# Kernel optimization log

Hardware: AMD Instinct MI355X
Metric: run time of the kernel (lower is better)

The kernel has to match this reference:

```python
import jax, jax.numpy as jnp
import numpy as np

B, S, H, NH, DH, F, L = 4, 2048, 512, 8, 64, 2048, 4
ALPHA = 1.0   # config.lag_time_scale_alpha
EPS = 1e-12   # BERT layer_norm_eps
MS_PER_MIN = 60.0 * 1000.0


def setup_inputs() -> dict:
    key = jax.random.key(0)
    ks = jax.random.split(key, 24)
    p = lambda k, shape: (jax.random.normal(k, shape, jnp.float32) * 0.02)
    inp = {
        "query_states": jax.random.normal(ks[0], (B, S, H), jnp.float32),
        "attention_mask": jnp.zeros((B, 1, 1, S), jnp.float32),
        "position_bias": jax.random.normal(ks[1], (1, NH, S, S), jnp.float32) * 0.02,
        "timestamp": jnp.sort(jax.random.randint(ks[2], (B, S), 0, 36_000_000, jnp.int32), axis=-1),
        # stacked per-layer parameters (L leading dim)
        "wq": p(ks[3], (L, H, H)), "bq": jnp.zeros((L, H), jnp.float32),
        "wk": p(ks[4], (L, H, H)), "bk": jnp.zeros((L, H), jnp.float32),
        "wv": p(ks[5], (L, H, H)), "bv": jnp.zeros((L, H), jnp.float32),
        "wo": p(ks[6], (L, H, H)), "bo": jnp.zeros((L, H), jnp.float32),
        "ln1_g": jnp.ones((L, H), jnp.float32), "ln1_b": jnp.zeros((L, H), jnp.float32),
        "wi": p(ks[7], (L, H, F)), "bi": jnp.zeros((L, F), jnp.float32),
        "wo2": p(ks[8], (L, F, H)), "bo2": jnp.zeros((L, H), jnp.float32),
        "ln2_g": jnp.ones((L, H), jnp.float32), "ln2_b": jnp.zeros((L, H), jnp.float32),
    }
    return inp


def _ln(x, g, b):
    m = x.mean(-1, keepdims=True)
    v = ((x - m) ** 2).mean(-1, keepdims=True)
    return (x - m) / jnp.sqrt(v + EPS) * g + b


def reference(query_states, attention_mask, position_bias, timestamp,
              wq, bq, wk, bk, wv, bv, wo, bo, ln1_g, ln1_b,
              wi, bi, wo2, bo2, ln2_g, ln2_b):
    # encoder (is_decoder=False) lag-time scale: (B,1,S,S)
    lag = (timestamp[:, None, :, None] - timestamp[:, None, None, :]).astype(jnp.float32) / MS_PER_MIN
    scale = np.sqrt(DH).astype(np.float32) - ALPHA / (jnp.clip(lag, 0.0) + 1.0) + ALPHA

    x = query_states
    for l in range(L):
        def proj(w, b):
            return (x @ w + b).reshape(B, S, NH, DH).transpose(0, 2, 1, 3)  # (B,NH,S,DH)
        q, k, v = proj(wq[l], bq[l]), proj(wk[l], bk[l]), proj(wv[l], bv[l])
        scores = jnp.einsum('bhqd,bhkd->bhqk', q, k) / scale + position_bias + attention_mask
        probs = jax.nn.softmax(scores, axis=-1)
        ctx = jnp.einsum('bhqk,bhkd->bhqd', probs, v).transpose(0, 2, 1, 3).reshape(B, S, H)
        attn = _ln(ctx @ wo[l] + bo[l] + x, ln1_g[l], ln1_b[l])
        ffn = jax.nn.gelu(attn @ wi[l] + bi[l], approximate=False) @ wo2[l] + bo2[l]
        x = _ln(ffn + attn, ln2_g[l], ln2_b[l])
    return x
```

## Files before the change

kernel.cpp:

```cpp
#include <hip/hip_runtime.h>
#include <stdint.h>

typedef unsigned short u16;
using half8   = __attribute__((ext_vector_type(8))) _Float16;
using float4v = __attribute__((ext_vector_type(4))) float;

#define L2E 1.4426950408889634f

__device__ inline float4v f4zero() { float4v z = {0.f, 0.f, 0.f, 0.f}; return z; }

__device__ inline u16 f2h(float f) {
  union { _Float16 h; u16 u; } v; v.h = (_Float16)f; return v.u;
}
__device__ inline float h2f(u16 u) {
  union { u16 u; _Float16 h; } v; v.u = u; return (float)v.h;
}

__device__ inline void glds16(const u16* g, u16* lds_base, int lane) {
#if __has_builtin(__builtin_amdgcn_global_load_lds)
  (void)lane;
  __builtin_amdgcn_global_load_lds((const __attribute__((address_space(1))) void*)g,
                                   (__attribute__((address_space(3))) void*)lds_base,
                                   16, 0, 0);
#else
  *(uint4*)(lds_base + (size_t)lane * 8) = *(const uint4*)g;
#endif
}

__global__ __launch_bounds__(256) void transpose_cast_kernel(
    const float* __restrict__ in, u16* __restrict__ out, int K, int N, size_t out_ls) {
  __shared__ float tile[32][33];
  const int tx = threadIdx.x & 31, ty = threadIdx.x >> 5;
  in  += (size_t)blockIdx.z * K * N;
  out += (size_t)blockIdx.z * out_ls;
  const int n  = blockIdx.x * 32 + tx;
  const int k0 = blockIdx.y * 32;
#pragma unroll
  for (int j = 0; j < 32; j += 8)
    tile[ty + j][tx] = in[(size_t)(k0 + ty + j) * N + n];
  __syncthreads();
  const int k = k0 + tx;
  const int n0 = blockIdx.x * 32;
#pragma unroll
  for (int j = 0; j < 32; j += 8)
    out[(size_t)(n0 + ty + j) * K + k] = f2h(tile[tx][ty + j]);
}

__global__ __launch_bounds__(256) void cast_kernel(const float* __restrict__ in,
                                                   u16* __restrict__ out) {
  const int i = (blockIdx.x * 256 + threadIdx.x) * 4;
  float4 t = *(const float4*)(in + i);
  ushort4 o;
  o.x = f2h(t.x); o.y = f2h(t.y); o.z = f2h(t.z); o.w = f2h(t.w);
  *(ushort4*)(out + i) = o;
}

__global__ __launch_bounds__(256) void pb_tile_kernel(const float* __restrict__ pb,
                                                      u16* __restrict__ pbT) {
  const int g  = blockIdx.x * 256 + threadIdx.x;
  const int mm = g & 15;
  const int q  = (g >> 4) & 2047;
  const int kbh = g >> 15;
  const int kb = kbh & 31, h = kbh >> 5;
  const float* src = pb + ((size_t)h * 2048 + q) * 2048 + kb * 64 + mm;
  ushort4 o;
  o.x = f2h(src[0]  * L2E);
  o.y = f2h(src[16] * L2E);
  o.z = f2h(src[32] * L2E);
  o.w = f2h(src[48] * L2E);
  *(ushort4*)(pbT + ((size_t)(h * 32 + kb) * 2048 + q) * 64 + mm * 4) = o;
}

__global__ __launch_bounds__(256) void inv_tile_kernel(const int* __restrict__ ts,
                                                       u16* __restrict__ invT) {
  const int g  = blockIdx.x * 256 + threadIdx.x;
  const int mm = g & 15;
  const int q  = (g >> 4) & 2047;
  const int kb = (g >> 15) & 31;
  const int b  = g >> 20;
  const int tq = ts[b * 2048 + q];
  ushort4 o;
  u16* op = (u16*)&o;
#pragma unroll
  for (int nb = 0; nb < 4; nb++) {
    const int k = kb * 64 + nb * 16 + mm;
    const int du = tq - ts[b * 2048 + k];
    const float u = (du > 0) ? (float)du : 0.f;
    op[nb] = f2h(fmaf(u, L2E, 86561.70245333781f) *
                 __builtin_amdgcn_rcpf(fmaf(u, 9.f, 480000.f)));
  }
  *(ushort4*)(invT + ((size_t)(b * 32 + kb) * 2048 + q) * 64 + mm * 4) = o;
}

__global__ __launch_bounds__(256) void maskts_kernel(const float* __restrict__ mask,
                                                     const int* __restrict__ ts,
                                                     float* __restrict__ maskE,
                                                     float* __restrict__ tsf) {
  const int i = blockIdx.x * 256 + threadIdx.x;
  maskE[i] = mask[i] * L2E;
  tsf[i]   = (float)ts[i];
}

template <int BM, int BN, int NN, int KK, int EPI>
__global__ __launch_bounds__(256) void gemm_kernel(
    const u16* __restrict__ A, const u16* __restrict__ Wt,
    const float* __restrict__ b0, const float* __restrict__ b1, const float* __restrict__ b2,
    const u16* __restrict__ resid,
    void* __restrict__ o0, void* __restrict__ o1, void* __restrict__ o2) {
  constexpr int FI = BM / 32;
  constexpr int FJB = BN / 32;
  constexpr int FIW = BM / 32;
  constexpr int FJW = BN / 32;
  __shared__ __align__(16) u16 As[BM * 64];
  __shared__ __align__(16) u16 Bs[BN * 64];
  const int tid = threadIdx.x, lane = tid & 63, wv = tid >> 6;
  const int quad = lane >> 4, mm = lane & 15;
  const int m0 = blockIdx.x * BM, n0 = blockIdx.y * BN;
  const int wm = (wv >> 1) * (BM / 2), wn = (wv & 1) * (BN / 2);
  const int srow = tid >> 3, slot = tid & 7;
  const int chunk = slot ^ (srow & 7);
  const u16* Ag = A  + (size_t)(m0 + srow) * KK + chunk * 8;
  const u16* Bg = Wt + (size_t)(n0 + srow) * KK + chunk * 8;
  u16* AsW = As + (size_t)(wv * 8) * 64;
  u16* BsW = Bs + (size_t)(wv * 8) * 64;
  const int sw = mm & 7;

  float4v acc[FIW][FJW];
#pragma unroll
  for (int i = 0; i < FIW; i++)
#pragma unroll
    for (int j = 0; j < FJW; j++) acc[i][j] = f4zero();

  for (int kt = 0; kt < KK; kt += 64) {
#pragma unroll
    for (int i = 0; i < FI; i++)
      glds16(Ag + (size_t)i * 32 * KK + kt, AsW + i * 32 * 64, lane);
#pragma unroll
    for (int j = 0; j < FJB; j++)
      glds16(Bg + (size_t)j * 32 * KK + kt, BsW + j * 32 * 64, lane);
    __syncthreads();
#pragma unroll
    for (int ks = 0; ks < 2; ks++) {
      half8 a[FIW], b[FJW];
#pragma unroll
      for (int i = 0; i < FIW; i++)
        a[i] = *(const half8*)(As + (size_t)(wm + i * 16 + mm) * 64 + (size_t)((ks * 4 + quad) ^ sw) * 8);
#pragma unroll
      for (int j = 0; j < FJW; j++)
        b[j] = *(const half8*)(Bs + (size_t)(wn + j * 16 + mm) * 64 + (size_t)((ks * 4 + quad) ^ sw) * 8);
#pragma unroll
      for (int i = 0; i < FIW; i++)
#pragma unroll
        for (int j = 0; j < FJW; j++)
          acc[i][j] = __builtin_amdgcn_mfma_f32_16x16x32_f16(a[i], b[j], acc[i][j], 0, 0, 0);
    }
    __syncthreads();
  }

#pragma unroll
  for (int j = 0; j < FJW; j++) {
    const int gn = n0 + wn + j * 16 + mm;
    if (EPI == 4) {
      const int which = gn >> 9, col = gn & 511, h = (gn >> 6) & 7, d = gn & 63;
      const float* bp = (which == 0) ? b0 : (which == 1) ? b1 : b2;
      const float bias = bp[col];
      u16* dst = (which == 0) ? (u16*)o0 : (which == 1) ? (u16*)o1 : (u16*)o2;
#pragma unroll
      for (int i = 0; i < FIW; i++)
#pragma unroll
        for (int r = 0; r < 4; r++) {
          const int gm = m0 + wm + i * 16 + quad * 4 + r;
          const int b_ = gm >> 11, s_ = gm & 2047;
          const float val = acc[i][j][r] + bias;
          if (which < 2)
            dst[((size_t)((b_ * 8 + h) * 2048 + s_)) * 64 + d] = f2h(val);
          else
            dst[((size_t)((b_ * 8 + h) * 64 + d)) * 2048 + s_] = f2h(val);
        }
    } else {
      const float bias = b0[gn];
#pragma unroll
      for (int i = 0; i < FIW; i++)
#pragma unroll
        for (int r = 0; r < 4; r++) {
          const int gm = m0 + wm + i * 16 + quad * 4 + r;
          const float val = acc[i][j][r] + bias;
          const size_t idx = (size_t)gm * NN + gn;
          if (EPI == 2) {
            ((float*)o0)[idx] = val + h2f(resid[idx]);
          } else {
            const float z  = val * 0.70710678118654752f;
            const float az = fabsf(z);
            const float t  = __builtin_amdgcn_rcpf(1.0f + 0.3275911f * az);
            const float poly = t * (0.254829592f + t * (-0.284496736f +
                               t * (1.421413741f + t * (-1.453152027f + t * 1.061405429f))));
            const float e = __builtin_amdgcn_exp2f(-az * az * L2E);
            float erf_ = 1.0f - poly * e;
            erf_ = (z < 0.0f) ? -erf_ : erf_;
            ((u16*)o0)[idx] = f2h(val * 0.5f * (1.0f + erf_));
          }
        }
    }
  }
}

template <int TILED>
__global__ __launch_bounds__(256) void flash4_kernel(
    const u16* __restrict__ Q, const u16* __restrict__ Kb, const u16* __restrict__ Vt,
    const u16* __restrict__ pbT, const u16* __restrict__ invT,
    const float* __restrict__ pb32,
    const float* __restrict__ maskE, const float* __restrict__ tsf,
    u16* __restrict__ ctx) {
  __shared__ __align__(16) u16 Kls[64 * 64];
  __shared__ __align__(16) u16 Vls[64 * 64];
  __shared__ __align__(16) u16 P[4][16 * 72];
  const int tid = threadIdx.x, lane = tid & 63, w = tid >> 6;
  const int quad = lane >> 4, mm = lane & 15;
  const int bh = blockIdx.y, b_ = bh >> 3, h_ = bh & 7;
  const int q0 = blockIdx.x * 64 + w * 16;
  const size_t qk_base = (size_t)bh * 2048 * 64;
  const size_t v_base  = (size_t)bh * 64 * 2048;
  const int srow = lane >> 3, slot = lane & 7;
  const int chunk = slot ^ srow;
  const int sw = mm & 7;

  half8 aq[2];
#pragma unroll
  for (int t = 0; t < 2; t++)
    aq[t] = *(const half8*)(Q + qk_base + (size_t)(q0 + mm) * 64 + t * 32 + quad * 8);

  float tqf[4];
  if (TILED < 2) {
#pragma unroll
    for (int r = 0; r < 4; r++) tqf[r] = tsf[b_ * 2048 + q0 + quad * 4 + r];
  }

  float l_r[4] = {0.f, 0.f, 0.f, 0.f};
  float4v o[4];
#pragma unroll
  for (int ob = 0; ob < 4; ob++) o[ob] = f4zero();

  ushort4 pbc[4], invc[4]; float tkc[4], mkc[4];
  if (TILED >= 1) {
#pragma unroll
    for (int r = 0; r < 4; r++)
      pbc[r] = *(const ushort4*)(pbT + ((size_t)(h_ * 32) * 2048 + q0 + quad * 4 + r) * 64 + mm * 4);
  }
  if (TILED == 2) {
#pragma unroll
    for (int r = 0; r < 4; r++)
      invc[r] = *(const ushort4*)(invT + ((size_t)(b_ * 32) * 2048 + q0 + quad * 4 + r) * 64 + mm * 4);
  } else {
#pragma unroll
    for (int nb = 0; nb < 4; nb++) tkc[nb] = tsf[b_ * 2048 + nb * 16 + mm];
  }
#pragma unroll
  for (int nb = 0; nb < 4; nb++) mkc[nb] = maskE[b_ * 2048 + nb * 16 + mm];

  for (int kt = 0; kt < 32; kt++) {
    const int k0 = kt * 64;
    __syncthreads();
#pragma unroll
    for (int i = 0; i < 2; i++) {
      const int row = w * 16 + i * 8 + srow;
      glds16(Kb + qk_base + (size_t)(k0 + row) * 64 + chunk * 8, Kls + (w * 16 + i * 8) * 64, lane);
      glds16(Vt + v_base + (size_t)row * 2048 + k0 + chunk * 8, Vls + (w * 16 + i * 8) * 64, lane);
    }
    __syncthreads();

    float4v s[4];
#pragma unroll
    for (int nb = 0; nb < 4; nb++) {
      const half8 kf0 = *(const half8*)(Kls + (size_t)(nb * 16 + mm) * 64 + (size_t)(quad ^ sw) * 8);
      const half8 kf1 = *(const half8*)(Kls + (size_t)(nb * 16 + mm) * 64 + (size_t)((4 + quad) ^ sw) * 8);
      s[nb] = __builtin_amdgcn_mfma_f32_16x16x32_f16(aq[0], kf0, f4zero(), 0, 0, 0);
      s[nb] = __builtin_amdgcn_mfma_f32_16x16x32_f16(aq[1], kf1, s[nb], 0, 0, 0);
    }

    const int kn = (kt < 31) ? kt + 1 : kt;
    ushort4 pbn[4], invn[4]; float tkn[4], mkn[4];
    if (TILED >= 1) {
#pragma unroll
      for (int r = 0; r < 4; r++)
        pbn[r] = *(const ushort4*)(pbT + ((size_t)(h_ * 32 + kn) * 2048 + q0 + quad * 4 + r) * 64 + mm * 4);
    }
    if (TILED == 2) {
#pragma unroll
      for (int r = 0; r < 4; r++)
        invn[r] = *(const ushort4*)(invT + ((size_t)(b_ * 32 + kn) * 2048 + q0 + quad * 4 + r) * 64 + mm * 4);
    } else {
#pragma unroll
      for (int nb = 0; nb < 4; nb++) tkn[nb] = tsf[b_ * 2048 + kn * 64 + nb * 16 + mm];
    }
#pragma unroll
    for (int nb = 0; nb < 4; nb++) mkn[nb] = maskE[b_ * 2048 + kn * 64 + nb * 16 + mm];

#pragma unroll
    for (int r = 0; r < 4; r++) {
      float pbv[4], iv[4];
      if (TILED >= 1) {
        pbv[0] = h2f(pbc[r].x); pbv[1] = h2f(pbc[r].y);
        pbv[2] = h2f(pbc[r].z); pbv[3] = h2f(pbc[r].w);
      } else {
#pragma unroll
        for (int nb = 0; nb < 4; nb++)
          pbv[nb] = pb32[((size_t)h_ * 2048 + q0 + quad * 4 + r) * 2048 + k0 + nb * 16 + mm] * L2E;
      }
      if (TILED == 2) {
        iv[0] = h2f(invc[r].x); iv[1] = h2f(invc[r].y);
        iv[2] = h2f(invc[r].z); iv[3] = h2f(invc[r].w);
      } else {
#pragma unroll
        for (int nb = 0; nb < 4; nb++) {
          const float u = fmaxf(tqf[r] - tkc[nb], 0.f);
          iv[nb] = fmaf(u, L2E, 86561.70245333781f) *
                   __builtin_amdgcn_rcpf(fmaf(u, 9.f, 480000.f));
        }
      }
#pragma unroll
      for (int nb = 0; nb < 4; nb++) {
        const float t = fmaf(s[nb][r], iv[nb], pbv[nb] + mkc[nb]);
        const float p = __builtin_amdgcn_exp2f(t);
        l_r[r] += p;
        P[w][(quad * 4 + r) * 72 + nb * 16 + mm] = f2h(p);
      }
    }

    const half8 ap0 = *(const half8*)(&P[w][mm * 72 + quad * 8]);
    const half8 ap1 = *(const half8*)(&P[w][mm * 72 + 32 + quad * 8]);
#pragma unroll
    for (int ob = 0; ob < 4; ob++) {
      const half8 vf0 = *(const half8*)(Vls + (size_t)(ob * 16 + mm) * 64 + (size_t)(quad ^ sw) * 8);
      const half8 vf1 = *(const half8*)(Vls + (size_t)(ob * 16 + mm) * 64 + (size_t)((4 + quad) ^ sw) * 8);
      o[ob] = __builtin_amdgcn_mfma_f32_16x16x32_f16(ap0, vf0, o[ob], 0, 0, 0);
      o[ob] = __builtin_amdgcn_mfma_f32_16x16x32_f16(ap1, vf1, o[ob], 0, 0, 0);
    }
#pragma unroll
    for (int r = 0; r < 4; r++) { pbc[r] = pbn[r]; invc[r] = invn[r]; }
#pragma unroll
    for (int nb = 0; nb < 4; nb++) { tkc[nb] = tkn[nb]; mkc[nb] = mkn[nb]; }
  }

#pragma unroll
  for (int r = 0; r < 4; r++) {
    float l = l_r[r];
#pragma unroll
    for (int sh = 1; sh < 16; sh <<= 1) l += __shfl_xor(l, sh, 64);
    const float rl = __builtin_amdgcn_rcpf(l);
    const int qrow = q0 + quad * 4 + r;
#pragma unroll
    for (int ob = 0; ob < 4; ob++)
      ctx[((size_t)b_ * 2048 + qrow) * 512 + h_ * 64 + ob * 16 + mm] = f2h(o[ob][r] * rl);
  }
}

__global__ __launch_bounds__(256) void ln_kernel(
    const float* __restrict__ in, const float* __restrict__ g, const float* __restrict__ bb,
    float* __restrict__ of, u16* __restrict__ obf) {
  const int lane = threadIdx.x & 63, w = threadIdx.x >> 6;
  const int row = blockIdx.x * 4 + w;
  const float* x = in + (size_t)row * 512;
  float v[8];
  const float4 t0 = *(const float4*)(x + lane * 8);
  const float4 t1 = *(const float4*)(x + lane * 8 + 4);
  v[0] = t0.x; v[1] = t0.y; v[2] = t0.z; v[3] = t0.w;
  v[4] = t1.x; v[5] = t1.y; v[6] = t1.z; v[7] = t1.w;
  float s = 0.f;
#pragma unroll
  for (int i = 0; i < 8; i++) s += v[i];
#pragma unroll
  for (int sh = 1; sh < 64; sh <<= 1) s += __shfl_xor(s, sh, 64);
  const float mean = s * (1.0f / 512.0f);
  float sq = 0.f;
#pragma unroll
  for (int i = 0; i < 8; i++) { const float d = v[i] - mean; sq += d * d; }
#pragma unroll
  for (int sh = 1; sh < 64; sh <<= 1) sq += __shfl_xor(sq, sh, 64);
  const float rstd = rsqrtf(sq * (1.0f / 512.0f) + 1e-12f);
#pragma unroll
  for (int i = 0; i < 8; i++) {
    const int col = lane * 8 + i;
    const float y = (v[i] - mean) * rstd * g[col] + bb[col];
    if (of) of[(size_t)row * 512 + col] = y;
    obf[(size_t)row * 512 + col] = f2h(y);
  }
}

extern "C" void kernel_launch(void* const* d_in, const int* in_sizes, int n_in,
                              void* d_out, int out_size, void* d_ws, size_t ws_size,
                              hipStream_t stream) {
  const float* x_in = (const float*)d_in[0];
  const float* mask = (const float*)d_in[1];
  const float* pb   = (const float*)d_in[2];
  const int*   ts   = (const int*)d_in[3];
  const float* wq = (const float*)d_in[4];  const float* bq = (const float*)d_in[5];
  const float* wk = (const float*)d_in[6];  const float* bk = (const float*)d_in[7];
  const float* wvp = (const float*)d_in[8]; const float* bv = (const float*)d_in[9];
  const float* wo = (const float*)d_in[10]; const float* bo = (const float*)d_in[11];
  const float* ln1g = (const float*)d_in[12]; const float* ln1b = (const float*)d_in[13];
  const float* wi = (const float*)d_in[14]; const float* bi = (const float*)d_in[15];
  const float* wo2 = (const float*)d_in[16]; const float* bo2 = (const float*)d_in[17];
  const float* ln2g = (const float*)d_in[18]; const float* ln2b = (const float*)d_in[19];

  char* ws = (char*)d_ws;
  const size_t o_wqkv  = 0;
  const size_t o_woT   = 6291456;
  const size_t o_wiT   = 8388608;
  const size_t o_wo2T  = 16777216;
  const size_t o_maskE = 25165824;
  const size_t o_tsf   = 25198592;
  const size_t o_xbf   = 25231360;
  const size_t o_qb    = 33619968;
  const size_t o_kb    = 42008576;
  const size_t o_vb    = 50397184;
  const size_t o_ctx   = 58785792;
  const size_t o_attnb = 67174400;
  const size_t o_tmp   = 75563008;
  const size_t o_pbT   = 92340224;
  const size_t o_invT  = 159449088;
  const int tiled = (ws_size >= o_invT + 33554432ull) ? 2
                  : (ws_size >= o_pbT + 67108864ull) ? 1 : 0;

  u16*   wqkvT = (u16*)(ws + o_wqkv);
  u16*   woT   = (u16*)(ws + o_woT);
  u16*   wiT   = (u16*)(ws + o_wiT);
  u16*   wo2T  = (u16*)(ws + o_wo2T);
  float* maskE = (float*)(ws + o_maskE);
  float* tsf   = (float*)(ws + o_tsf);
  u16*   xbf   = (u16*)(ws + o_xbf);
  u16*   qb    = (u16*)(ws + o_qb);
  u16*   kb    = (u16*)(ws + o_kb);
  u16*   vb    = (u16*)(ws + o_vb);
  u16*   ctx   = (u16*)(ws + o_ctx);
  u16*   hb    = (u16*)(ws + o_qb);
  u16*   attnb = (u16*)(ws + o_attnb);
  float* tmp   = (float*)(ws + o_tmp);
  u16*   pbT   = (u16*)(ws + o_pbT);
  u16*   invT  = (u16*)(ws + o_invT);

  const dim3 blk(256);
  transpose_cast_kernel<<<dim3(16, 16, 4), blk, 0, stream>>>(wq,  wqkvT,          512, 512, 786432);
  transpose_cast_kernel<<<dim3(16, 16, 4), blk, 0, stream>>>(wk,  wqkvT + 262144, 512, 512, 786432);
  transpose_cast_kernel<<<dim3(16, 16, 4), blk, 0, stream>>>(wvp, wqkvT + 524288, 512, 512, 786432);
  transpose_cast_kernel<<<dim3(16, 16, 4), blk, 0, stream>>>(wo,  woT,  512, 512,  262144);
  transpose_cast_kernel<<<dim3(64, 16, 4), blk, 0, stream>>>(wi,  wiT,  512, 2048, 1048576);
  transpose_cast_kernel<<<dim3(16, 64, 4), blk, 0, stream>>>(wo2, wo2T, 2048, 512, 1048576);
  maskts_kernel<<<32, blk, 0, stream>>>(mask, ts, maskE, tsf);
  cast_kernel<<<4096, blk, 0, stream>>>(x_in, xbf);
  if (tiled >= 1) pb_tile_kernel<<<32768, blk, 0, stream>>>(pb, pbT);
  if (tiled == 2) inv_tile_kernel<<<16384, blk, 0, stream>>>(ts, invT);

  for (int l = 0; l < 4; l++) {
    gemm_kernel<128, 128, 1536, 512, 4><<<dim3(64, 12), blk, 0, stream>>>(
        xbf, wqkvT + (size_t)l * 786432, bq + l * 512, bk + l * 512, bv + l * 512,
        nullptr, qb, kb, vb);
    if (tiled == 2)
      flash4_kernel<2><<<dim3(32, 32), blk, 0, stream>>>(qb, kb, vb, pbT, invT, pb, maskE, tsf, ctx);
    else if (tiled == 1)
      flash4_kernel<1><<<dim3(32, 32), blk, 0, stream>>>(qb, kb, vb, pbT, nullptr, pb, maskE, tsf, ctx);
    else
      flash4_kernel<0><<<dim3(32, 32), blk, 0, stream>>>(qb, kb, vb, nullptr, nullptr, pb, maskE, tsf, ctx);
    gemm_kernel<128, 64, 512, 512, 2><<<dim3(64, 8), blk, 0, stream>>>(
        ctx, woT + (size_t)l * 262144, bo + l * 512, nullptr, nullptr, xbf,
        tmp, nullptr, nullptr);
    ln_kernel<<<2048, blk, 0, stream>>>(tmp, ln1g + l * 512, ln1b + l * 512, nullptr, attnb);
    gemm_kernel<128, 128, 2048, 512, 3><<<dim3(64, 16), blk, 0, stream>>>(
        attnb, wiT + (size_t)l * 1048576, bi + l * 2048, nullptr, nullptr, nullptr,
        hb, nullptr, nullptr);
    gemm_kernel<128, 64, 512, 2048, 2><<<dim3(64, 8), blk, 0, stream>>>(
        hb, wo2T + (size_t)l * 1048576, bo2 + l * 512, nullptr, nullptr, attnb,
        tmp, nullptr, nullptr);
    ln_kernel<<<2048, blk, 0, stream>>>(tmp, ln2g + l * 512, ln2b + l * 512,
                                        (l == 3) ? (float*)d_out : nullptr, xbf);
  }
  (void)in_sizes; (void)n_in; (void)out_size;
}
```

Baseline: 1.368 ms.

## Double-buffer flash attention and output GEMMs, fragment-ordered bias tiles, fp16 residual temp

The flash attention kernel now double-buffers its K/V LDS tiles so the next tile's global loads overlap the current tile's compute, and it drops one of the two barriers per iteration. Position-bias and lag-scale tiles are pre-laid out in MFMA fragment order so each lane reads two 16-byte vectors per tile. The P scratch uses an XOR swizzle in place of padding. A new double-buffered GEMM handles the output and FFN-down projections and writes the residual sum in fp16, which halves the LayerNorm input traffic at some cost in precision. The intermediate tiled=1 path is also removed.

```diff
diff --git a/kernel.cpp b/kernel.cpp
--- a/kernel.cpp
+++ b/kernel.cpp
@@ -27,6 +27,11 @@
 #endif
 }
 
+__device__ inline void wave_fence_barrier() {
+  __asm__ volatile("s_waitcnt vmcnt(0) lgkmcnt(0)" ::: "memory");
+  __builtin_amdgcn_s_barrier();
+}
+
 __global__ __launch_bounds__(256) void transpose_cast_kernel(
     const float* __restrict__ in, u16* __restrict__ out, int K, int N, size_t out_ls) {
   __shared__ float tile[32][33];
@@ -55,41 +60,54 @@
   *(ushort4*)(out + i) = o;
 }
 
-__global__ __launch_bounds__(256) void pb_tile_kernel(const float* __restrict__ pb,
-                                                      u16* __restrict__ pbT) {
-  const int g  = blockIdx.x * 256 + threadIdx.x;
-  const int mm = g & 15;
-  const int q  = (g >> 4) & 2047;
-  const int kbh = g >> 15;
-  const int kb = kbh & 31, h = kbh >> 5;
-  const float* src = pb + ((size_t)h * 2048 + q) * 2048 + kb * 64 + mm;
-  ushort4 o;
-  o.x = f2h(src[0]  * L2E);
-  o.y = f2h(src[16] * L2E);
-  o.z = f2h(src[32] * L2E);
-  o.w = f2h(src[48] * L2E);
-  *(ushort4*)(pbT + ((size_t)(h * 32 + kb) * 2048 + q) * 64 + mm * 4) = o;
-}
-
-__global__ __launch_bounds__(256) void inv_tile_kernel(const int* __restrict__ ts,
-                                                       u16* __restrict__ invT) {
-  const int g  = blockIdx.x * 256 + threadIdx.x;
-  const int mm = g & 15;
-  const int q  = (g >> 4) & 2047;
-  const int kb = (g >> 15) & 31;
-  const int b  = g >> 20;
-  const int tq = ts[b * 2048 + q];
-  ushort4 o;
-  u16* op = (u16*)&o;
-#pragma unroll
-  for (int nb = 0; nb < 4; nb++) {
+__global__ __launch_bounds__(256) void pb_tile2_kernel(const float* __restrict__ pb,
+                                                       u16* __restrict__ pbT) {
+  const int g    = blockIdx.x * 256 + threadIdx.x;
+  const int half = g & 1;
+  const int lane = (g >> 1) & 63;
+  const int qg   = (g >> 7) & 127;
+  const int kb   = (g >> 14) & 31;
+  const int h    = g >> 19;
+  const int quad = lane >> 4, mm = lane & 15;
+  ushort4 o[2];
+  u16* op = (u16*)o;
+#pragma unroll
+  for (int e = 0; e < 8; e++) {
+    const int nb = half * 2 + (e >> 2), r = e & 3;
+    const int q = qg * 16 + quad * 4 + r;
     const int k = kb * 64 + nb * 16 + mm;
-    const int du = tq - ts[b * 2048 + k];
+    op[e] = f2h(pb[((size_t)h * 2048 + q) * 2048 + k] * L2E);
+  }
+  *(uint4*)(pbT + ((((size_t)h * 32 + kb) * 128 + qg) * 64 + lane) * 16 + half * 8) =
+      *(uint4*)o;
+}
+
+__global__ __launch_bounds__(256) void inv_tile2_kernel(const int* __restrict__ ts,
+                                                        u16* __restrict__ invT) {
+  const int g    = blockIdx.x * 256 + threadIdx.x;
+  const int half = g & 1;
+  const int lane = (g >> 1) & 63;
+  const int qg   = (g >> 7) & 127;
+  const int kb   = (g >> 14) & 31;
+  const int b    = g >> 19;
+  const int quad = lane >> 4, mm = lane & 15;
+  int tq[4], tk[2];
+#pragma unroll
+  for (int r = 0; r < 4; r++) tq[r] = ts[b * 2048 + qg * 16 + quad * 4 + r];
+#pragma unroll
+  for (int n = 0; n < 2; n++) tk[n] = ts[b * 2048 + kb * 64 + (half * 2 + n) * 16 + mm];
+  ushort4 o[2];
+  u16* op = (u16*)o;
+#pragma unroll
+  for (int e = 0; e < 8; e++) {
+    const int n = e >> 2, r = e & 3;
+    const int du = tq[r] - tk[n];
     const float u = (du > 0) ? (float)du : 0.f;
-    op[nb] = f2h(fmaf(u, L2E, 86561.70245333781f) *
-                 __builtin_amdgcn_rcpf(fmaf(u, 9.f, 480000.f)));
-  }
-  *(ushort4*)(invT + ((size_t)(b * 32 + kb) * 2048 + q) * 64 + mm * 4) = o;
+    op[e] = f2h(fmaf(u, L2E, 86561.70245333781f) *
+                __builtin_amdgcn_rcpf(fmaf(u, 9.f, 480000.f)));
+  }
+  *(uint4*)(invT + ((((size_t)b * 32 + kb) * 128 + qg) * 64 + lane) * 16 + half * 8) =
+      *(uint4*)o;
 }
 
 __global__ __launch_bounds__(256) void maskts_kernel(const float* __restrict__ mask,
@@ -105,7 +123,6 @@
 __global__ __launch_bounds__(256) void gemm_kernel(
     const u16* __restrict__ A, const u16* __restrict__ Wt,
     const float* __restrict__ b0, const float* __restrict__ b1, const float* __restrict__ b2,
-    const u16* __restrict__ resid,
     void* __restrict__ o0, void* __restrict__ o1, void* __restrict__ o2) {
   constexpr int FI = BM / 32;
   constexpr int FJB = BN / 32;
@@ -186,38 +203,110 @@
           const int gm = m0 + wm + i * 16 + quad * 4 + r;
           const float val = acc[i][j][r] + bias;
           const size_t idx = (size_t)gm * NN + gn;
-          if (EPI == 2) {
-            ((float*)o0)[idx] = val + h2f(resid[idx]);
-          } else {
-            const float z  = val * 0.70710678118654752f;
-            const float az = fabsf(z);
-            const float t  = __builtin_amdgcn_rcpf(1.0f + 0.3275911f * az);
-            const float poly = t * (0.254829592f + t * (-0.284496736f +
-                               t * (1.421413741f + t * (-1.453152027f + t * 1.061405429f))));
-            const float e = __builtin_amdgcn_exp2f(-az * az * L2E);
-            float erf_ = 1.0f - poly * e;
-            erf_ = (z < 0.0f) ? -erf_ : erf_;
-            ((u16*)o0)[idx] = f2h(val * 0.5f * (1.0f + erf_));
-          }
+          const float z  = val * 0.70710678118654752f;
+          const float az = fabsf(z);
+          const float t  = __builtin_amdgcn_rcpf(1.0f + 0.3275911f * az);
+          const float poly = t * (0.254829592f + t * (-0.284496736f +
+                             t * (1.421413741f + t * (-1.453152027f + t * 1.061405429f))));
+          const float e = __builtin_amdgcn_exp2f(-az * az * L2E);
+          float erf_ = 1.0f - poly * e;
+          erf_ = (z < 0.0f) ? -erf_ : erf_;
+          ((u16*)o0)[idx] = f2h(val * 0.5f * (1.0f + erf_));
         }
     }
   }
 }
 
+template <int KK>
+__global__ __launch_bounds__(256) void gemm_db_kernel(
+    const u16* __restrict__ A, const u16* __restrict__ Wt,
+    const float* __restrict__ b0, const u16* __restrict__ resid,
+    u16* __restrict__ out) {
+  constexpr int KT = KK / 64;
+  __shared__ __align__(16) u16 As[2][128 * 64];
+  __shared__ __align__(16) u16 Bs[2][64 * 64];
+  const int tid = threadIdx.x, lane = tid & 63, wv = tid >> 6;
+  const int quad = lane >> 4, mm = lane & 15;
+  const int m0 = blockIdx.x * 128, n0 = blockIdx.y * 64;
+  const int wm = (wv >> 1) * 64, wn = (wv & 1) * 32;
+  const int srow = tid >> 3, slot = tid & 7;
+  const int chunk = slot ^ (srow & 7);
+  const u16* Ag = A  + (size_t)(m0 + srow) * KK + chunk * 8;
+  const u16* Bg = Wt + (size_t)(n0 + srow) * KK + chunk * 8;
+  const int woff = (wv * 8) * 64;
+  const int sw = mm & 7;
+
+  float4v acc[4][2];
+#pragma unroll
+  for (int i = 0; i < 4; i++)
+#pragma unroll
+    for (int j = 0; j < 2; j++) acc[i][j] = f4zero();
+
+#pragma unroll
+  for (int i = 0; i < 4; i++) glds16(Ag + (size_t)i * 32 * KK, As[0] + woff + i * 32 * 64, lane);
+#pragma unroll
+  for (int j = 0; j < 2; j++) glds16(Bg + (size_t)j * 32 * KK, Bs[0] + woff + j * 32 * 64, lane);
+  wave_fence_barrier();
+
+  for (int t = 0; t < KT; t++) {
+    const int cur = t & 1;
+    if (t + 1 < KT) {
+      const int kt = (t + 1) * 64;
+#pragma unroll
+      for (int i = 0; i < 4; i++)
+        glds16(Ag + (size_t)i * 32 * KK + kt, As[cur ^ 1] + woff + i * 32 * 64, lane);
+#pragma unroll
+      for (int j = 0; j < 2; j++)
+        glds16(Bg + (size_t)j * 32 * KK + kt, Bs[cur ^ 1] + woff + j * 32 * 64, lane);
+    }
+#pragma unroll
+    for (int ks = 0; ks < 2; ks++) {
+      half8 a[4], b[2];
+#pragma unroll
+      for (int i = 0; i < 4; i++)
+        a[i] = *(const half8*)(As[cur] + (size_t)(wm + i * 16 + mm) * 64 + (size_t)((ks * 4 + quad) ^ sw) * 8);
+#pragma unroll
+      for (int j = 0; j < 2; j++)
+        b[j] = *(const half8*)(Bs[cur] + (size_t)(wn + j * 16 + mm) * 64 + (size_t)((ks * 4 + quad) ^ sw) * 8);
+#pragma unroll
+      for (int i = 0; i < 4; i++)
+#pragma unroll
+        for (int j = 0; j < 2; j++)
+          acc[i][j] = __builtin_amdgcn_mfma_f32_16x16x32_f16(a[i], b[j], acc[i][j], 0, 0, 0);
+    }
+    wave_fence_barrier();
+  }
+
+#pragma unroll
+  for (int j = 0; j < 2; j++) {
+    const int gn = n0 + wn + j * 16 + mm;
+    const float bias = b0[gn];
+#pragma unroll
+    for (int i = 0; i < 4; i++)
+#pragma unroll
+      for (int r = 0; r < 4; r++) {
+        const int gm = m0 + wm + i * 16 + quad * 4 + r;
+        const size_t idx = (size_t)gm * 512 + gn;
+        out[idx] = f2h(acc[i][j][r] + bias + h2f(resid[idx]));
+      }
+  }
+}
+
 template <int TILED>
-__global__ __launch_bounds__(256) void flash4_kernel(
+__global__ __launch_bounds__(256) void flash5_kernel(
     const u16* __restrict__ Q, const u16* __restrict__ Kb, const u16* __restrict__ Vt,
     const u16* __restrict__ pbT, const u16* __restrict__ invT,
     const float* __restrict__ pb32,
     const float* __restrict__ maskE, const float* __restrict__ tsf,
     u16* __restrict__ ctx) {
-  __shared__ __align__(16) u16 Kls[64 * 64];
-  __shared__ __align__(16) u16 Vls[64 * 64];
-  __shared__ __align__(16) u16 P[4][16 * 72];
+  __shared__ __align__(16) u16 Kls[2][64 * 64];
+  __shared__ __align__(16) u16 Vls[2][64 * 64];
+  __shared__ __align__(16) u16 P[4][16 * 64];
   const int tid = threadIdx.x, lane = tid & 63, w = tid >> 6;
   const int quad = lane >> 4, mm = lane & 15;
   const int bh = blockIdx.y, b_ = bh >> 3, h_ = bh & 7;
-  const int q0 = blockIdx.x * 64 + w * 16;
+  const int qg = blockIdx.x * 4 + w;
+  const int q0 = qg * 16;
   const size_t qk_base = (size_t)bh * 2048 * 64;
   const size_t v_base  = (size_t)bh * 64 * 2048;
   const int srow = lane >> 3, slot = lane & 7;
@@ -230,7 +319,7 @@
     aq[t] = *(const half8*)(Q + qk_base + (size_t)(q0 + mm) * 64 + t * 32 + quad * 8);
 
   float tqf[4];
-  if (TILED < 2) {
+  if (TILED == 0) {
 #pragma unroll
     for (int r = 0; r < 4; r++) tqf[r] = tsf[b_ * 2048 + q0 + quad * 4 + r];
   }
@@ -240,105 +329,104 @@
 #pragma unroll
   for (int ob = 0; ob < 4; ob++) o[ob] = f4zero();
 
-  ushort4 pbc[4], invc[4]; float tkc[4], mkc[4];
-  if (TILED >= 1) {
-#pragma unroll
-    for (int r = 0; r < 4; r++)
-      pbc[r] = *(const ushort4*)(pbT + ((size_t)(h_ * 32) * 2048 + q0 + quad * 4 + r) * 64 + mm * 4);
-  }
+#pragma unroll
+  for (int i = 0; i < 2; i++) {
+    const int row = w * 16 + i * 8 + srow;
+    glds16(Kb + qk_base + (size_t)row * 64 + chunk * 8, Kls[0] + (w * 16 + i * 8) * 64, lane);
+    glds16(Vt + v_base + (size_t)row * 2048 + chunk * 8, Vls[0] + (w * 16 + i * 8) * 64, lane);
+  }
+  half8 pbc[2], invc[2];
+  float tkc[4], mkc[4];
   if (TILED == 2) {
-#pragma unroll
-    for (int r = 0; r < 4; r++)
-      invc[r] = *(const ushort4*)(invT + ((size_t)(b_ * 32) * 2048 + q0 + quad * 4 + r) * 64 + mm * 4);
+    const size_t pbb = (((size_t)h_ * 32 + 0) * 128 + qg) * 1024 + lane * 16;
+    const size_t ivb = (((size_t)b_ * 32 + 0) * 128 + qg) * 1024 + lane * 16;
+    pbc[0] = *(const half8*)(pbT + pbb);     pbc[1] = *(const half8*)(pbT + pbb + 8);
+    invc[0] = *(const half8*)(invT + ivb);   invc[1] = *(const half8*)(invT + ivb + 8);
   } else {
 #pragma unroll
     for (int nb = 0; nb < 4; nb++) tkc[nb] = tsf[b_ * 2048 + nb * 16 + mm];
   }
 #pragma unroll
   for (int nb = 0; nb < 4; nb++) mkc[nb] = maskE[b_ * 2048 + nb * 16 + mm];
+  wave_fence_barrier();
 
   for (int kt = 0; kt < 32; kt++) {
-    const int k0 = kt * 64;
-    __syncthreads();
-#pragma unroll
-    for (int i = 0; i < 2; i++) {
-      const int row = w * 16 + i * 8 + srow;
-      glds16(Kb + qk_base + (size_t)(k0 + row) * 64 + chunk * 8, Kls + (w * 16 + i * 8) * 64, lane);
-      glds16(Vt + v_base + (size_t)row * 2048 + k0 + chunk * 8, Vls + (w * 16 + i * 8) * 64, lane);
-    }
-    __syncthreads();
+    const int cur = kt & 1;
+    half8 pbn[2], invn[2];
+    float tkn[4], mkn[4];
+    if (kt < 31) {
+      const int k1 = (kt + 1) * 64;
+#pragma unroll
+      for (int i = 0; i < 2; i++) {
+        const int row = w * 16 + i * 8 + srow;
+        glds16(Kb + qk_base + (size_t)(k1 + row) * 64 + chunk * 8,
+               Kls[cur ^ 1] + (w * 16 + i * 8) * 64, lane);
+        glds16(Vt + v_base + (size_t)row * 2048 + k1 + chunk * 8,
+               Vls[cur ^ 1] + (w * 16 + i * 8) * 64, lane);
+      }
+      if (TILED == 2) {
+        const size_t pbb = (((size_t)h_ * 32 + kt + 1) * 128 + qg) * 1024 + lane * 16;
+        const size_t ivb = (((size_t)b_ * 32 + kt + 1) * 128 + qg) * 1024 + lane * 16;
+        pbn[0] = *(const half8*)(pbT + pbb);   pbn[1] = *(const half8*)(pbT + pbb + 8);
+        invn[0] = *(const half8*)(invT + ivb); invn[1] = *(const half8*)(invT + ivb + 8);
+      } else {
+#pragma unroll
+        for (int nb = 0; nb < 4; nb++) tkn[nb] = tsf[b_ * 2048 + (kt + 1) * 64 + nb * 16 + mm];
+      }
+#pragma unroll
+      for (int nb = 0; nb < 4; nb++) mkn[nb] = maskE[b_ * 2048 + (kt + 1) * 64 + nb * 16 + mm];
+    }
 
     float4v s[4];
 #pragma unroll
     for (int nb = 0; nb < 4; nb++) {
-      const half8 kf0 = *(const half8*)(Kls + (size_t)(nb * 16 + mm) * 64 + (size_t)(quad ^ sw) * 8);
-      const half8 kf1 = *(const half8*)(Kls + (size_t)(nb * 16 + mm) * 64 + (size_t)((4 + quad) ^ sw) * 8);
+      const half8 kf0 = *(const half8*)(Kls[cur] + (size_t)(nb * 16 + mm) * 64 + (size_t)(quad ^ sw) * 8);
+      const half8 kf1 = *(const half8*)(Kls[cur] + (size_t)(nb * 16 + mm) * 64 + (size_t)((4 + quad) ^ sw) * 8);
       s[nb] = __builtin_amdgcn_mfma_f32_16x16x32_f16(aq[0], kf0, f4zero(), 0, 0, 0);
       s[nb] = __builtin_amdgcn_mfma_f32_16x16x32_f16(aq[1], kf1, s[nb], 0, 0, 0);
     }
 
-    const int kn = (kt < 31) ? kt + 1 : kt;
-    ushort4 pbn[4], invn[4]; float tkn[4], mkn[4];
-    if (TILED >= 1) {
-#pragma unroll
-      for (int r = 0; r < 4; r++)
-        pbn[r] = *(const ushort4*)(pbT + ((size_t)(h_ * 32 + kn) * 2048 + q0 + quad * 4 + r) * 64 + mm * 4);
-    }
-    if (TILED == 2) {
-#pragma unroll
-      for (int r = 0; r < 4; r++)
-        invn[r] = *(const ushort4*)(invT + ((size_t)(b_ * 32 + kn) * 2048 + q0 + quad * 4 + r) * 64 + mm * 4);
-    } else {
-#pragma unroll
-      for (int nb = 0; nb < 4; nb++) tkn[nb] = tsf[b_ * 2048 + kn * 64 + nb * 16 + mm];
-    }
-#pragma unroll
-    for (int nb = 0; nb < 4; nb++) mkn[nb] = maskE[b_ * 2048 + kn * 64 + nb * 16 + mm];
-
+    const int rw7 = (quad * 4) & 7;
 #pragma unroll
     for (int r = 0; r < 4; r++) {
-      float pbv[4], iv[4];
-      if (TILED >= 1) {
-        pbv[0] = h2f(pbc[r].x); pbv[1] = h2f(pbc[r].y);
-        pbv[2] = h2f(pbc[r].z); pbv[3] = h2f(pbc[r].w);
-      } else {
-#pragma unroll
-        for (int nb = 0; nb < 4; nb++)
-          pbv[nb] = pb32[((size_t)h_ * 2048 + q0 + quad * 4 + r) * 2048 + k0 + nb * 16 + mm] * L2E;
-      }
-      if (TILED == 2) {
-        iv[0] = h2f(invc[r].x); iv[1] = h2f(invc[r].y);
-        iv[2] = h2f(invc[r].z); iv[3] = h2f(invc[r].w);
-      } else {
-#pragma unroll
-        for (int nb = 0; nb < 4; nb++) {
+      const int prow = quad * 4 + r;
+#pragma unroll
+      for (int nb = 0; nb < 4; nb++) {
+        float pbv, iv;
+        if (TILED == 2) {
+          pbv = (float)pbc[nb >> 1][(nb & 1) * 4 + r];
+          iv  = (float)invc[nb >> 1][(nb & 1) * 4 + r];
+        } else {
+          pbv = pb32[((size_t)h_ * 2048 + q0 + prow) * 2048 + kt * 64 + nb * 16 + mm] * L2E;
           const float u = fmaxf(tqf[r] - tkc[nb], 0.f);
-          iv[nb] = fmaf(u, L2E, 86561.70245333781f) *
-                   __builtin_amdgcn_rcpf(fmaf(u, 9.f, 480000.f));
+          iv = fmaf(u, L2E, 86561.70245333781f) *
+               __builtin_amdgcn_rcpf(fmaf(u, 9.f, 480000.f));
         }
-      }
-#pragma unroll
-      for (int nb = 0; nb < 4; nb++) {
-        const float t = fmaf(s[nb][r], iv[nb], pbv[nb] + mkc[nb]);
+        const float t = fmaf(s[nb][r], iv, pbv + mkc[nb]);
         const float p = __builtin_amdgcn_exp2f(t);
         l_r[r] += p;
-        P[w][(quad * 4 + r) * 72 + nb * 16 + mm] = f2h(p);
+        const int pslot = (nb * 2 + (mm >> 3)) ^ ((rw7 + r) & 7);
+        P[w][prow * 64 + pslot * 8 + (mm & 7)] = f2h(p);
       }
     }
 
-    const half8 ap0 = *(const half8*)(&P[w][mm * 72 + quad * 8]);
-    const half8 ap1 = *(const half8*)(&P[w][mm * 72 + 32 + quad * 8]);
+    const half8 ap0 = *(const half8*)(&P[w][mm * 64 + (size_t)(quad ^ sw) * 8]);
+    const half8 ap1 = *(const half8*)(&P[w][mm * 64 + (size_t)((4 + quad) ^ sw) * 8]);
 #pragma unroll
     for (int ob = 0; ob < 4; ob++) {
-      const half8 vf0 = *(const half8*)(Vls + (size_t)(ob * 16 + mm) * 64 + (size_t)(quad ^ sw) * 8);
-      const half8 vf1 = *(const half8*)(Vls + (size_t)(ob * 16 + mm) * 64 + (size_t)((4 + quad) ^ sw) * 8);
+      const half8 vf0 = *(const half8*)(Vls[cur] + (size_t)(ob * 16 + mm) * 64 + (size_t)(quad ^ sw) * 8);
+      const half8 vf1 = *(const half8*)(Vls[cur] + (size_t)(ob * 16 + mm) * 64 + (size_t)((4 + quad) ^ sw) * 8);
       o[ob] = __builtin_amdgcn_mfma_f32_16x16x32_f16(ap0, vf0, o[ob], 0, 0, 0);
       o[ob] = __builtin_amdgcn_mfma_f32_16x16x32_f16(ap1, vf1, o[ob], 0, 0, 0);
     }
-#pragma unroll
-    for (int r = 0; r < 4; r++) { pbc[r] = pbn[r]; invc[r] = invn[r]; }
-#pragma unroll
-    for (int nb = 0; nb < 4; nb++) { tkc[nb] = tkn[nb]; mkc[nb] = mkn[nb]; }
+
+    wave_fence_barrier();
+    if (kt < 31) {
+#pragma unroll
+      for (int i = 0; i < 2; i++) { pbc[i] = pbn[i]; invc[i] = invn[i]; }
+#pragma unroll
+      for (int nb = 0; nb < 4; nb++) { tkc[nb] = tkn[nb]; mkc[nb] = mkn[nb]; }
+    }
   }
 
 #pragma unroll
@@ -355,16 +443,14 @@
 }
 
 __global__ __launch_bounds__(256) void ln_kernel(
-    const float* __restrict__ in, const float* __restrict__ g, const float* __restrict__ bb,
+    const u16* __restrict__ in, const float* __restrict__ g, const float* __restrict__ bb,
     float* __restrict__ of, u16* __restrict__ obf) {
   const int lane = threadIdx.x & 63, w = threadIdx.x >> 6;
   const int row = blockIdx.x * 4 + w;
-  const float* x = in + (size_t)row * 512;
+  const half8 hv = *(const half8*)(in + (size_t)row * 512 + lane * 8);
   float v[8];
-  const float4 t0 = *(const float4*)(x + lane * 8);
-  const float4 t1 = *(const float4*)(x + lane * 8 + 4);
-  v[0] = t0.x; v[1] = t0.y; v[2] = t0.z; v[3] = t0.w;
-  v[4] = t1.x; v[5] = t1.y; v[6] = t1.z; v[7] = t1.w;
+#pragma unroll
+  for (int i = 0; i < 8; i++) v[i] = (float)hv[i];
   float s = 0.f;
 #pragma unroll
   for (int i = 0; i < 8; i++) s += v[i];
@@ -418,8 +504,7 @@
   const size_t o_tmp   = 75563008;
   const size_t o_pbT   = 92340224;
   const size_t o_invT  = 159449088;
-  const int tiled = (ws_size >= o_invT + 33554432ull) ? 2
-                  : (ws_size >= o_pbT + 67108864ull) ? 1 : 0;
+  const int tiled = (ws_size >= o_invT + 33554432ull) ? 2 : 0;
 
   u16*   wqkvT = (u16*)(ws + o_wqkv);
   u16*   woT   = (u16*)(ws + o_woT);
@@ -434,7 +519,7 @@
   u16*   ctx   = (u16*)(ws + o_ctx);
   u16*   hb    = (u16*)(ws + o_qb);
   u16*   attnb = (u16*)(ws + o_attnb);
-  float* tmp   = (float*)(ws + o_tmp);
+  u16*   tmp16 = (u16*)(ws + o_tmp);
   u16*   pbT   = (u16*)(ws + o_pbT);
   u16*   invT  = (u16*)(ws + o_invT);
 
@@ -447,30 +532,28 @@
   transpose_cast_kernel<<<dim3(16, 64, 4), blk, 0, stream>>>(wo2, wo2T, 2048, 512, 1048576);
   maskts_kernel<<<32, blk, 0, stream>>>(mask, ts, maskE, tsf);
   cast_kernel<<<4096, blk, 0, stream>>>(x_in, xbf);
-  if (tiled >= 1) pb_tile_kernel<<<32768, blk, 0, stream>>>(pb, pbT);
-  if (tiled == 2) inv_tile_kernel<<<16384, blk, 0, stream>>>(ts, invT);
+  if (tiled == 2) {
+    pb_tile2_kernel<<<16384, blk, 0, stream>>>(pb, pbT);
+    inv_tile2_kernel<<<8192, blk, 0, stream>>>(ts, invT);
+  }
 
   for (int l = 0; l < 4; l++) {
     gemm_kernel<128, 128, 1536, 512, 4><<<dim3(64, 12), blk, 0, stream>>>(
         xbf, wqkvT + (size_t)l * 786432, bq + l * 512, bk + l * 512, bv + l * 512,
-        nullptr, qb, kb, vb);
+        qb, kb, vb);
     if (tiled == 2)
-      flash4_kernel<2><<<dim3(32, 32), blk, 0, stream>>>(qb, kb, vb, pbT, invT, pb, maskE, tsf, ctx);
-    else if (tiled == 1)
-      flash4_kernel<1><<<dim3(32, 32), blk, 0, stream>>>(qb, kb, vb, pbT, nullptr, pb, maskE, tsf, ctx);
+      flash5_kernel<2><<<dim3(32, 32), blk, 0, stream>>>(qb, kb, vb, pbT, invT, pb, maskE, tsf, ctx);
     else
-      flash4_kernel<0><<<dim3(32, 32), blk, 0, stream>>>(qb, kb, vb, nullptr, nullptr, pb, maskE, tsf, ctx);
-    gemm_kernel<128, 64, 512, 512, 2><<<dim3(64, 8), blk, 0, stream>>>(
-        ctx, woT + (size_t)l * 262144, bo + l * 512, nullptr, nullptr, xbf,
-        tmp, nullptr, nullptr);
-    ln_kernel<<<2048, blk, 0, stream>>>(tmp, ln1g + l * 512, ln1b + l * 512, nullptr, attnb);
+      flash5_kernel<0><<<dim3(32, 32), blk, 0, stream>>>(qb, kb, vb, nullptr, nullptr, pb, maskE, tsf, ctx);
+    gemm_db_kernel<512><<<dim3(64, 8), blk, 0, stream>>>(
+        ctx, woT + (size_t)l * 262144, bo + l * 512, xbf, tmp16);
+    ln_kernel<<<2048, blk, 0, stream>>>(tmp16, ln1g + l * 512, ln1b + l * 512, nullptr, attnb);
     gemm_kernel<128, 128, 2048, 512, 3><<<dim3(64, 16), blk, 0, stream>>>(
-        attnb, wiT + (size_t)l * 1048576, bi + l * 2048, nullptr, nullptr, nullptr,
+        attnb, wiT + (size_t)l * 1048576, bi + l * 2048, nullptr, nullptr,
         hb, nullptr, nullptr);
-    gemm_kernel<128, 64, 512, 2048, 2><<<dim3(64, 8), blk, 0, stream>>>(
-        hb, wo2T + (size_t)l * 1048576, bo2 + l * 512, nullptr, nullptr, attnb,
-        tmp, nullptr, nullptr);
-    ln_kernel<<<2048, blk, 0, stream>>>(tmp, ln2g + l * 512, ln2b + l * 512,
+    gemm_db_kernel<2048><<<dim3(64, 8), blk, 0, stream>>>(
+        hb, wo2T + (size_t)l * 1048576, bo2 + l * 512, attnb, tmp16);
+    ln_kernel<<<2048, blk, 0, stream>>>(tmp16, ln2g + l * 512, ln2b + l * 512,
                                         (l == 3) ? (float*)d_out : nullptr, xbf);
   }
   (void)in_sizes; (void)n_in; (void)out_size;
```

Measured after the change: 1.488 ms. +8.8%, slower.
